# Kernel tuning notes

Measured on AMD Instinct MI355X. Metric: run time of the kernel, lower is better.

Reference implementation:

```python
import jax, jax.numpy as jnp
import numpy as np

D_IN = 512
D_OUT = 512
EPS = 1e-5


def setup_inputs() -> dict:
    key = jax.random.key(0)
    ks = jax.random.split(key, 6)
    B, T = 256, D_OUT + 1  # T includes CLS token (dropped in forward)
    x = jax.random.normal(ks[0], (B, T, D_IN), dtype=jnp.float32)
    s = 1.0 / np.sqrt(D_IN)
    W1 = jax.random.uniform(ks[1], (D_IN, D_IN), jnp.float32, -s, s)
    b1 = jax.random.uniform(ks[2], (D_IN,), jnp.float32, -s, s)
    gamma = jnp.ones((D_IN,), jnp.float32)
    beta = jnp.zeros((D_IN,), jnp.float32)
    Wout = jax.random.uniform(ks[3], (D_OUT, D_IN), jnp.float32, -s, s)  # stacked per-column Linear(d_in,1) weights
    bout = jax.random.uniform(ks[4], (D_OUT,), jnp.float32, -s, s)
    return {"x": x, "W1": W1, "b1": b1, "gamma": gamma, "beta": beta,
            "Wout": Wout, "bout": bout}


def reference(x, W1, b1, gamma, beta, Wout, bout):
    h = x[:, :-1]                              # drop CLS: [B, d_out, d_in]
    h = jnp.einsum('btd,ed->bte', h, W1) + b1  # linear1
    mu = jnp.mean(h, axis=-1, keepdims=True)
    var = jnp.mean(jnp.square(h - mu), axis=-1, keepdims=True)
    h = (h - mu) * jax.lax.rsqrt(var + EPS) * gamma + beta  # LayerNorm
    h = jax.nn.relu(h)
    # per-column head: out[:, t] = h[:, t] @ Wout[t] + bout[t]
    out = jnp.einsum('btd,td->bt', h, Wout) + bout  # [B, d_out]
    return out
```

## Files before the change

kernel.cpp:

```cpp
#include <hip/hip_runtime.h>


#define DIN     512
#define BK      32
#define MT      128
#define THREADS 1024
#define NCHUNK  (DIN / BK)
#define ASTR    40
#define BROW    32

typedef __attribute__((ext_vector_type(8))) short bf16x8;
typedef __attribute__((ext_vector_type(4))) float f32x4;

__device__ __forceinline__ short f2bf(float f) {
    unsigned u = __float_as_uint(f);
    u = u + 0x7fffu + ((u >> 16) & 1u);
    return (short)(u >> 16);
}

__device__ __forceinline__ void gload_lds16(const void* g, void* l) {
    __builtin_amdgcn_global_load_lds(
        (const __attribute__((address_space(1))) unsigned int*)g,
        (__attribute__((address_space(3))) unsigned int*)l,
        16, 0, 0);
}

__global__ void cvt_w1_kernel(const float* __restrict__ w, short* __restrict__ o) {
    int i = blockIdx.x * blockDim.x + threadIdx.x;
    float4 v = ((const float4*)w)[i];
    short4 s;
    s.x = f2bf(v.x); s.y = f2bf(v.y); s.z = f2bf(v.z); s.w = f2bf(v.w);
    ((short4*)o)[i] = s;
}

__device__ __forceinline__ void stage_b_f32(short* bsb, const float* W1f,
                                            int c, int tid) {
    if (tid < DIN) {
        const float* src = W1f + (size_t)tid * DIN + c * BK;
        const int rp = tid & 3;
#pragma unroll
        for (int g = 0; g < 4; ++g) {
            float4 v0 = *(const float4*)(src + g * 8);
            float4 v1 = *(const float4*)(src + g * 8 + 4);
            bf16x8 s;
            s[0] = f2bf(v0.x); s[1] = f2bf(v0.y); s[2] = f2bf(v0.z); s[3] = f2bf(v0.w);
            s[4] = f2bf(v1.x); s[5] = f2bf(v1.y); s[6] = f2bf(v1.z); s[7] = f2bf(v1.w);
            *(bf16x8*)(bsb + tid * BROW + ((g ^ rp) * 8)) = s;
        }
    }
}

template<bool WS>
__global__ __launch_bounds__(THREADS)
void fused_head_kernel(const float* __restrict__ x,
                       const float* __restrict__ W1f,
                       const short* __restrict__ W1h,
                       const float* __restrict__ b1,
                       const float* __restrict__ gamma,
                       const float* __restrict__ beta,
                       const float* __restrict__ Wout,
                       const float* __restrict__ bout,
                       float* __restrict__ out) {
    __shared__ __align__(16) short As[2][MT * ASTR];
    __shared__ __align__(16) short Bs[2][DIN * BROW];
    __shared__ float redS[MT][4];
    __shared__ float redQ[MT][4];
    __shared__ float meanA[MT];
    __shared__ float rstdA[MT];

    const int tid  = threadIdx.x;
    const int w    = tid >> 6;
    const int lane = tid & 63;
    const int q    = lane >> 4;
    const int l15  = lane & 15;
    const int rg   = w >> 2;
    const int cg   = w & 3;

    const int m0 = blockIdx.x * MT;
    const int bb = m0 >> 9;
    const int t0 = m0 & 511;
    const float* xbase = x + (size_t)(bb * 513 + t0) * DIN;

    const int ar = tid >> 3;
    const int ak = (tid & 7) * 4;

    const int r16 = lane >> 2;
    const int kg  = (lane & 3) ^ (r16 & 3);
    const short* bG = W1h + (size_t)(w * 32 + r16) * DIN + kg * 8;

    f32x4 acc[2][8];
#pragma unroll
    for (int i = 0; i < 2; ++i)
#pragma unroll
        for (int j = 0; j < 8; ++j)
            acc[i][j] = (f32x4){0.f, 0.f, 0.f, 0.f};

    float4 aReg = *(const float4*)(xbase + ar * DIN + ak);
    if (WS) {
        gload_lds16(bG,            &Bs[0][(w * 32) * BROW]);
        gload_lds16(bG + 16 * DIN, &Bs[0][(w * 32 + 16) * BROW]);
    } else {
        stage_b_f32(&Bs[0][0], W1f, 0, tid);
    }
    {
        short4 a4;
        a4.x = f2bf(aReg.x); a4.y = f2bf(aReg.y);
        a4.z = f2bf(aReg.z); a4.w = f2bf(aReg.w);
        *(short4*)(&As[0][ar * ASTR + ak]) = a4;
    }
    aReg = *(const float4*)(xbase + ar * DIN + BK + ak);

    for (int c = 0; c < NCHUNK; ++c) {
        const int cur = c & 1, nxt = cur ^ 1;
        __syncthreads();
        if (c + 1 < NCHUNK) {
            if (WS) {
                const short* g = bG + (size_t)(c + 1) * BK;
                gload_lds16(g,            &Bs[nxt][(w * 32) * BROW]);
                gload_lds16(g + 16 * DIN, &Bs[nxt][(w * 32 + 16) * BROW]);
            } else {
                stage_b_f32(&Bs[nxt][0], W1f, c + 1, tid);
            }
            short4 a4;
            a4.x = f2bf(aReg.x); a4.y = f2bf(aReg.y);
            a4.z = f2bf(aReg.z); a4.w = f2bf(aReg.w);
            *(short4*)(&As[nxt][ar * ASTR + ak]) = a4;
            if (c + 2 < NCHUNK)
                aReg = *(const float4*)(xbase + ar * DIN + (c + 2) * BK + ak);
        }
        bf16x8 af[2];
        const short* Ap = &As[cur][(rg * 32 + l15) * ASTR + q * 8];
        af[0] = *(const bf16x8*)Ap;
        af[1] = *(const bf16x8*)(Ap + 16 * ASTR);
        const short* Bp = &Bs[cur][(cg * 128 + l15) * BROW + ((q ^ (l15 & 3)) * 8)];
#pragma unroll
        for (int tj = 0; tj < 8; ++tj) {
            bf16x8 bf = *(const bf16x8*)(Bp + tj * 16 * BROW);
            acc[0][tj] = __builtin_amdgcn_mfma_f32_16x16x32_bf16(af[0], bf, acc[0][tj], 0, 0, 0);
            acc[1][tj] = __builtin_amdgcn_mfma_f32_16x16x32_bf16(af[1], bf, acc[1][tj], 0, 0, 0);
        }
    }

    float b1v[8], gv[8], bv[8];
    const int cb = cg * 128 + l15;
#pragma unroll
    for (int tj = 0; tj < 8; ++tj) {
        int col = cb + tj * 16;
        b1v[tj] = b1[col];
        gv[tj]  = gamma[col];
        bv[tj]  = beta[col];
    }

#pragma unroll
    for (int ti = 0; ti < 2; ++ti)
#pragma unroll
        for (int r = 0; r < 4; ++r) {
            int row = rg * 32 + ti * 16 + q * 4 + r;
            float s = 0.f, s2 = 0.f;
#pragma unroll
            for (int tj = 0; tj < 8; ++tj) {
                float v = acc[ti][tj][r] + b1v[tj];
                s += v; s2 += v * v;
            }
#pragma unroll
            for (int m = 1; m < 16; m <<= 1) {
                s  += __shfl_xor(s,  m, 64);
                s2 += __shfl_xor(s2, m, 64);
            }
            if (l15 == 0) { redS[row][cg] = s; redQ[row][cg] = s2; }
        }
    __syncthreads();
    if (tid < MT) {
        float s  = redS[tid][0] + redS[tid][1] + redS[tid][2] + redS[tid][3];
        float s2 = redQ[tid][0] + redQ[tid][1] + redQ[tid][2] + redQ[tid][3];
        float mean = s * (1.f / DIN);
        float var  = s2 * (1.f / DIN) - mean * mean;
        meanA[tid] = mean;
        rstdA[tid] = rsqrtf(fmaxf(var, 0.f) + 1e-5f);
    }
    __syncthreads();

#pragma unroll
    for (int ti = 0; ti < 2; ++ti)
#pragma unroll
        for (int r = 0; r < 4; ++r) {
            int row = rg * 32 + ti * 16 + q * 4 + r;
            float mean = meanA[row], rs = rstdA[row];
            const float* wrow = Wout + (size_t)(t0 + row) * DIN + cb;
            float s = 0.f;
#pragma unroll
            for (int tj = 0; tj < 8; ++tj) {
                float v = acc[ti][tj][r] + b1v[tj];
                v = (v - mean) * rs * gv[tj] + bv[tj];
                v = fmaxf(v, 0.f);
                s += v * wrow[tj * 16];
            }
#pragma unroll
            for (int m = 1; m < 16; m <<= 1)
                s += __shfl_xor(s, m, 64);
            if (l15 == 0) redS[row][cg] = s;
        }
    __syncthreads();
    if (tid < MT)
        out[m0 + tid] = redS[tid][0] + redS[tid][1] + redS[tid][2] + redS[tid][3]
                        + bout[t0 + tid];
}

extern "C" void kernel_launch(void* const* d_in, const int* in_sizes, int n_in,
                              void* d_out, int out_size, void* d_ws, size_t ws_size,
                              hipStream_t stream) {
    const float* x     = (const float*)d_in[0];
    const float* W1    = (const float*)d_in[1];
    const float* b1    = (const float*)d_in[2];
    const float* gamma = (const float*)d_in[3];
    const float* beta  = (const float*)d_in[4];
    const float* Wout  = (const float*)d_in[5];
    const float* bout  = (const float*)d_in[6];
    float* out = (float*)d_out;

    const int M = 256 * 512;
    dim3 grid(M / MT), block(THREADS);

    if (ws_size >= (size_t)(DIN * DIN) * sizeof(short)) {
        short* W1h = (short*)d_ws;
        cvt_w1_kernel<<<DIN * DIN / (256 * 4), 256, 0, stream>>>(W1, W1h);
        fused_head_kernel<true><<<grid, block, 0, stream>>>(
            x, W1, W1h, b1, gamma, beta, Wout, bout, out);
    } else {
        fused_head_kernel<false><<<grid, block, 0, stream>>>(
            x, W1, nullptr, b1, gamma, beta, Wout, bout, out);
    }
}
```

Baseline: 446.2 us.

## Shrink block to 64 rows with 4 waves each owning 128 columns

The block tile drops from 128 rows on 16 waves to 64 rows on 4 waves, with launch bounds asking for 2 blocks per CU. Each wave now computes 64x128 of the output with four A fragments. This raises MFMA count per LDS fragment load and lets two blocks overlap their barriers. Staging of B changes to match, and the XOR swizzle on B in LDS is removed. The cost is twice as many blocks, each re-reading the whole bf16 W1 from L2, plus higher register pressure from the larger accumulator.

```diff
diff --git a/kernel.cpp b/kernel.cpp
--- a/kernel.cpp
+++ b/kernel.cpp
@@ -3,8 +3,8 @@
 
 #define DIN     512
 #define BK      32
-#define MT      128
-#define THREADS 1024
+#define MT      64
+#define THREADS 256
 #define NCHUNK  (DIN / BK)
 #define ASTR    40
 #define BROW    32
@@ -35,23 +35,24 @@
 
 __device__ __forceinline__ void stage_b_f32(short* bsb, const float* W1f,
                                             int c, int tid) {
-    if (tid < DIN) {
-        const float* src = W1f + (size_t)tid * DIN + c * BK;
-        const int rp = tid & 3;
-#pragma unroll
-        for (int g = 0; g < 4; ++g) {
+#pragma unroll
+    for (int h = 0; h < 2; ++h) {
+        int row = tid * 2 + h;
+        const float* src = W1f + (size_t)row * DIN + c * BK;
+#pragma unroll
+        for (int g = 0; g < 2; ++g) {
             float4 v0 = *(const float4*)(src + g * 8);
             float4 v1 = *(const float4*)(src + g * 8 + 4);
             bf16x8 s;
             s[0] = f2bf(v0.x); s[1] = f2bf(v0.y); s[2] = f2bf(v0.z); s[3] = f2bf(v0.w);
             s[4] = f2bf(v1.x); s[5] = f2bf(v1.y); s[6] = f2bf(v1.z); s[7] = f2bf(v1.w);
-            *(bf16x8*)(bsb + tid * BROW + ((g ^ rp) * 8)) = s;
+            *(bf16x8*)(bsb + row * BROW + g * 8) = s;
         }
     }
 }
 
 template<bool WS>
-__global__ __launch_bounds__(THREADS)
+__global__ __launch_bounds__(THREADS, 2)
 void fused_head_kernel(const float* __restrict__ x,
                        const float* __restrict__ W1f,
                        const short* __restrict__ W1h,
@@ -73,42 +74,42 @@
     const int lane = tid & 63;
     const int q    = lane >> 4;
     const int l15  = lane & 15;
-    const int rg   = w >> 2;
-    const int cg   = w & 3;
 
     const int m0 = blockIdx.x * MT;
     const int bb = m0 >> 9;
     const int t0 = m0 & 511;
     const float* xbase = x + (size_t)(bb * 513 + t0) * DIN;
 
-    const int ar = tid >> 3;
-    const int ak = (tid & 7) * 4;
-
-    const int r16 = lane >> 2;
-    const int kg  = (lane & 3) ^ (r16 & 3);
-    const short* bG = W1h + (size_t)(w * 32 + r16) * DIN + kg * 8;
-
-    f32x4 acc[2][8];
-#pragma unroll
-    for (int i = 0; i < 2; ++i)
+    const int ar = tid >> 2;
+    const int ak = (tid & 3) * 8;
+
+    const short* bG = W1h + (size_t)(w * 128 + (lane >> 2)) * DIN + (lane & 3) * 8;
+
+    f32x4 acc[4][8];
+#pragma unroll
+    for (int i = 0; i < 4; ++i)
 #pragma unroll
         for (int j = 0; j < 8; ++j)
             acc[i][j] = (f32x4){0.f, 0.f, 0.f, 0.f};
 
-    float4 aReg = *(const float4*)(xbase + ar * DIN + ak);
+    float4 a0 = *(const float4*)(xbase + ar * DIN + ak);
+    float4 a1 = *(const float4*)(xbase + ar * DIN + ak + 4);
     if (WS) {
-        gload_lds16(bG,            &Bs[0][(w * 32) * BROW]);
-        gload_lds16(bG + 16 * DIN, &Bs[0][(w * 32 + 16) * BROW]);
+#pragma unroll
+        for (int j = 0; j < 8; ++j)
+            gload_lds16(bG + (size_t)(j * 16) * DIN,
+                        &Bs[0][(w * 128 + j * 16) * BROW]);
     } else {
         stage_b_f32(&Bs[0][0], W1f, 0, tid);
     }
     {
-        short4 a4;
-        a4.x = f2bf(aReg.x); a4.y = f2bf(aReg.y);
-        a4.z = f2bf(aReg.z); a4.w = f2bf(aReg.w);
-        *(short4*)(&As[0][ar * ASTR + ak]) = a4;
-    }
-    aReg = *(const float4*)(xbase + ar * DIN + BK + ak);
+        bf16x8 s;
+        s[0] = f2bf(a0.x); s[1] = f2bf(a0.y); s[2] = f2bf(a0.z); s[3] = f2bf(a0.w);
+        s[4] = f2bf(a1.x); s[5] = f2bf(a1.y); s[6] = f2bf(a1.z); s[7] = f2bf(a1.w);
+        *(bf16x8*)(&As[0][ar * ASTR + ak]) = s;
+    }
+    a0 = *(const float4*)(xbase + ar * DIN + BK + ak);
+    a1 = *(const float4*)(xbase + ar * DIN + BK + ak + 4);
 
     for (int c = 0; c < NCHUNK; ++c) {
         const int cur = c & 1, nxt = cur ^ 1;
@@ -116,33 +117,40 @@
         if (c + 1 < NCHUNK) {
             if (WS) {
                 const short* g = bG + (size_t)(c + 1) * BK;
-                gload_lds16(g,            &Bs[nxt][(w * 32) * BROW]);
-                gload_lds16(g + 16 * DIN, &Bs[nxt][(w * 32 + 16) * BROW]);
+#pragma unroll
+                for (int j = 0; j < 8; ++j)
+                    gload_lds16(g + (size_t)(j * 16) * DIN,
+                                &Bs[nxt][(w * 128 + j * 16) * BROW]);
             } else {
                 stage_b_f32(&Bs[nxt][0], W1f, c + 1, tid);
             }
-            short4 a4;
-            a4.x = f2bf(aReg.x); a4.y = f2bf(aReg.y);
-            a4.z = f2bf(aReg.z); a4.w = f2bf(aReg.w);
-            *(short4*)(&As[nxt][ar * ASTR + ak]) = a4;
-            if (c + 2 < NCHUNK)
-                aReg = *(const float4*)(xbase + ar * DIN + (c + 2) * BK + ak);
-        }
-        bf16x8 af[2];
-        const short* Ap = &As[cur][(rg * 32 + l15) * ASTR + q * 8];
-        af[0] = *(const bf16x8*)Ap;
-        af[1] = *(const bf16x8*)(Ap + 16 * ASTR);
-        const short* Bp = &Bs[cur][(cg * 128 + l15) * BROW + ((q ^ (l15 & 3)) * 8)];
+            bf16x8 s;
+            s[0] = f2bf(a0.x); s[1] = f2bf(a0.y); s[2] = f2bf(a0.z); s[3] = f2bf(a0.w);
+            s[4] = f2bf(a1.x); s[5] = f2bf(a1.y); s[6] = f2bf(a1.z); s[7] = f2bf(a1.w);
+            *(bf16x8*)(&As[nxt][ar * ASTR + ak]) = s;
+            if (c + 2 < NCHUNK) {
+                a0 = *(const float4*)(xbase + ar * DIN + (c + 2) * BK + ak);
+                a1 = *(const float4*)(xbase + ar * DIN + (c + 2) * BK + ak + 4);
+            }
+        }
+        bf16x8 af[4];
+        const short* Ap = &As[cur][l15 * ASTR + q * 8];
+#pragma unroll
+        for (int ti = 0; ti < 4; ++ti)
+            af[ti] = *(const bf16x8*)(Ap + ti * 16 * ASTR);
+        const short* Bp = &Bs[cur][(w * 128 + l15) * BROW + q * 8];
 #pragma unroll
         for (int tj = 0; tj < 8; ++tj) {
             bf16x8 bf = *(const bf16x8*)(Bp + tj * 16 * BROW);
-            acc[0][tj] = __builtin_amdgcn_mfma_f32_16x16x32_bf16(af[0], bf, acc[0][tj], 0, 0, 0);
-            acc[1][tj] = __builtin_amdgcn_mfma_f32_16x16x32_bf16(af[1], bf, acc[1][tj], 0, 0, 0);
+#pragma unroll
+            for (int ti = 0; ti < 4; ++ti)
+                acc[ti][tj] = __builtin_amdgcn_mfma_f32_16x16x32_bf16(
+                    af[ti], bf, acc[ti][tj], 0, 0, 0);
         }
     }
 
     float b1v[8], gv[8], bv[8];
-    const int cb = cg * 128 + l15;
+    const int cb = w * 128 + l15;
 #pragma unroll
     for (int tj = 0; tj < 8; ++tj) {
         int col = cb + tj * 16;
@@ -152,10 +160,10 @@
     }
 
 #pragma unroll
-    for (int ti = 0; ti < 2; ++ti)
+    for (int ti = 0; ti < 4; ++ti)
 #pragma unroll
         for (int r = 0; r < 4; ++r) {
-            int row = rg * 32 + ti * 16 + q * 4 + r;
+            int row = ti * 16 + q * 4 + r;
             float s = 0.f, s2 = 0.f;
 #pragma unroll
             for (int tj = 0; tj < 8; ++tj) {
@@ -167,7 +175,7 @@
                 s  += __shfl_xor(s,  m, 64);
                 s2 += __shfl_xor(s2, m, 64);
             }
-            if (l15 == 0) { redS[row][cg] = s; redQ[row][cg] = s2; }
+            if (l15 == 0) { redS[row][w] = s; redQ[row][w] = s2; }
         }
     __syncthreads();
     if (tid < MT) {
@@ -181,10 +189,10 @@
     __syncthreads();
 
 #pragma unroll
-    for (int ti = 0; ti < 2; ++ti)
+    for (int ti = 0; ti < 4; ++ti)
 #pragma unroll
         for (int r = 0; r < 4; ++r) {
-            int row = rg * 32 + ti * 16 + q * 4 + r;
+            int row = ti * 16 + q * 4 + r;
             float mean = meanA[row], rs = rstdA[row];
             const float* wrow = Wout + (size_t)(t0 + row) * DIN + cb;
             float s = 0.f;
@@ -198,7 +206,7 @@
 #pragma unroll
             for (int m = 1; m < 16; m <<= 1)
                 s += __shfl_xor(s, m, 64);
-            if (l15 == 0) redS[row][cg] = s;
+            if (l15 == 0) redS[row][w] = s;
         }
     __syncthreads();
     if (tid < MT)
```

Result: no change. 447.7 us (+0.3%).
